# Performance work log

Measured on AMD Instinct MI355X. Metric: run time of the kernel, lower is better.

Reference implementation:

```python
import jax, jax.numpy as jnp
import numpy as np

DIM = 4096
HIDDEN = 11008
B, S = 4, 2048


def setup_inputs() -> dict:
    key = jax.random.key(0)
    k_x, k_g, k_u, k_d = jax.random.split(key, 4)
    x = jax.random.normal(k_x, (B, S, DIM), dtype=jnp.float32)
    # int8-range quantized weights, stored as int32 per spec (values in [-127, 127])
    w_gate = jax.random.randint(k_g, (HIDDEN, DIM), -127, 128, dtype=jnp.int32)
    w_up = jax.random.randint(k_u, (HIDDEN, DIM), -127, 128, dtype=jnp.int32)
    w_down = jax.random.randint(k_d, (DIM, HIDDEN), -127, 128, dtype=jnp.int32)
    # per-tensor scales (realistic small magnitudes)
    scale_gate = jnp.float32(0.01)
    scale_up = jnp.float32(0.01)
    scale_down = jnp.float32(0.01)
    return {
        "x": x,
        "w_gate": w_gate,
        "w_up": w_up,
        "w_down": w_down,
        "scale_gate": scale_gate,
        "scale_up": scale_up,
        "scale_down": scale_down,
    }


def _qlinear(x, w_int, scale):
    # faithful to QuantizedLinear.forward: dequantize then F.linear (x @ w.T)
    w = w_int.astype(x.dtype) * scale
    return jnp.einsum("bsd,hd->bsh", x, w)


def reference(x, w_gate, w_up, w_down, scale_gate, scale_up, scale_down):
    x_gate = _qlinear(x, w_gate, scale_gate)      # [B,S,HIDDEN]
    x_up = _qlinear(x, w_up, scale_up)            # [B,S,HIDDEN]
    x_mid = jax.nn.silu(x_gate) * x_up            # SwiGLU
    x_out = _qlinear(x_mid, w_down, scale_down)   # [B,S,DIM]
    return x_out
```

## Files before the change

kernel.cpp:

```cpp
#include <hip/hip_runtime.h>
#include <hip/hip_bf16.h>
#include <cstdint>
#include <cstddef>

#define DIM 4096
#define HIDDEN 11008
#define MTOK 8192

typedef __bf16 bf16x8 __attribute__((ext_vector_type(8)));
typedef float floatx4 __attribute__((ext_vector_type(4)));

__device__ __forceinline__ unsigned short f2bf(float f) {
    union { float f; unsigned int u; } v; v.f = f;
    unsigned int r = v.u + 0x7FFFu + ((v.u >> 16) & 1u);
    return (unsigned short)(r >> 16);
}

__device__ __forceinline__ void gload16(const void* g, void* l) {
    __builtin_amdgcn_global_load_lds(
        (const __attribute__((address_space(1))) unsigned int*)g,
        (__attribute__((address_space(3))) unsigned int*)l,
        16, 0, 0);
}

__device__ __forceinline__ floatx4 mfma16(bf16x8 a, bf16x8 b, floatx4 c) {
    return __builtin_amdgcn_mfma_f32_16x16x32_bf16(a, b, c, 0, 0, 0);
}


__global__ void cvt_f32_bf16(const float4* __restrict__ in, ushort4* __restrict__ out, int n4) {
    int i = blockIdx.x * 256 + threadIdx.x;
    if (i < n4) {
        float4 v = in[i];
        ushort4 o;
        o.x = f2bf(v.x); o.y = f2bf(v.y); o.z = f2bf(v.z); o.w = f2bf(v.w);
        out[i] = o;
    }
}

__global__ void cvt_i32_bf16(const int4* __restrict__ in, ushort4* __restrict__ out, int n4) {
    int i = blockIdx.x * 256 + threadIdx.x;
    if (i < n4) {
        int4 v = in[i];
        ushort4 o;
        o.x = f2bf((float)v.x); o.y = f2bf((float)v.y);
        o.z = f2bf((float)v.z); o.w = f2bf((float)v.w);
        out[i] = o;
    }
}

__global__ __launch_bounds__(256) void gemm_gateup(
    const unsigned short* __restrict__ A,
    const unsigned short* __restrict__ Bg,
    const unsigned short* __restrict__ Bu,
    unsigned short* __restrict__ mid,
    const float* __restrict__ sgp, const float* __restrict__ sup)
{
    __shared__ __align__(16) unsigned short sA[128 * 32];
    __shared__ __align__(16) unsigned short sBg[64 * 32];
    __shared__ __align__(16) unsigned short sBu[64 * 32];

    const int tid  = threadIdx.x;
    const int lane = tid & 63;
    const int wave = tid >> 6;
    const int wr   = wave >> 1;
    const int wc   = wave & 1;
    const int quad = lane >> 4;
    const int l16  = lane & 15;

    const size_t m0 = (size_t)blockIdx.x * 128;
    const size_t n0 = (size_t)blockIdx.y * 64;

    const int srow = tid >> 2;
    const int scol = (tid & 3) * 8;

    const unsigned short* gA0 = A  + (m0 + srow) * DIM + scol;
    const unsigned short* gA1 = gA0 + (size_t)64 * DIM;
    const unsigned short* gBg = Bg + (n0 + srow) * DIM + scol;
    const unsigned short* gBu = Bu + (n0 + srow) * DIM + scol;

    unsigned short* lA0 = &sA[tid * 8];
    unsigned short* lA1 = &sA[(tid + 256) * 8];
    unsigned short* lBg = &sBg[tid * 8];
    unsigned short* lBu = &sBu[tid * 8];

    const unsigned short* rA[4];
    const unsigned short* rBg[2];
    const unsigned short* rBu[2];
    for (int i = 0; i < 4; ++i)
        rA[i] = &sA[(wr * 64 + i * 16 + l16) * 32 + quad * 8];
    for (int j = 0; j < 2; ++j) {
        rBg[j] = &sBg[(wc * 32 + j * 16 + l16) * 32 + quad * 8];
        rBu[j] = &sBu[(wc * 32 + j * 16 + l16) * 32 + quad * 8];
    }

    floatx4 accg[4][2], accu[4][2];
    const floatx4 zero = {0.f, 0.f, 0.f, 0.f};
    for (int i = 0; i < 4; ++i)
        for (int j = 0; j < 2; ++j) { accg[i][j] = zero; accu[i][j] = zero; }

    for (int kt = 0; kt < DIM / 32; ++kt) {
        __syncthreads();
        gload16(gA0, lA0);
        gload16(gA1, lA1);
        gload16(gBg, lBg);
        gload16(gBu, lBu);
        gA0 += 32; gA1 += 32; gBg += 32; gBu += 32;
        __syncthreads();

        bf16x8 af[4], bg[2], bu[2];
        for (int i = 0; i < 4; ++i) af[i] = *(const bf16x8*)rA[i];
        for (int j = 0; j < 2; ++j) {
            bg[j] = *(const bf16x8*)rBg[j];
            bu[j] = *(const bf16x8*)rBu[j];
        }
        for (int i = 0; i < 4; ++i)
            for (int j = 0; j < 2; ++j) {
                accg[i][j] = mfma16(af[i], bg[j], accg[i][j]);
                accu[i][j] = mfma16(af[i], bu[j], accu[i][j]);
            }
    }

    const float s_g = *sgp;
    const float s_u = *sup;
    for (int i = 0; i < 4; ++i) {
        const size_t row = m0 + wr * 64 + i * 16 + quad * 4;
        for (int j = 0; j < 2; ++j) {
            const size_t col = n0 + wc * 32 + j * 16 + l16;
            for (int r = 0; r < 4; ++r) {
                float g = accg[i][j][r] * s_g;
                float u = accu[i][j][r] * s_u;
                float sig = 1.0f / (1.0f + __expf(-g));
                float v = g * sig * u;
                mid[(row + r) * HIDDEN + col] = f2bf(v);
            }
        }
    }
}

__global__ __launch_bounds__(256) void gemm_down(
    const unsigned short* __restrict__ A,
    const unsigned short* __restrict__ B,
    float* __restrict__ out,
    const float* __restrict__ sdp)
{
    __shared__ __align__(16) unsigned short sA[128 * 32];
    __shared__ __align__(16) unsigned short sB[128 * 32];

    const int tid  = threadIdx.x;
    const int lane = tid & 63;
    const int wave = tid >> 6;
    const int wr   = wave >> 1;
    const int wc   = wave & 1;
    const int quad = lane >> 4;
    const int l16  = lane & 15;

    const size_t m0 = (size_t)blockIdx.x * 128;
    const size_t n0 = (size_t)blockIdx.y * 128;

    const int srow = tid >> 2;
    const int scol = (tid & 3) * 8;

    const unsigned short* gA0 = A + (m0 + srow) * HIDDEN + scol;
    const unsigned short* gA1 = gA0 + (size_t)64 * HIDDEN;
    const unsigned short* gB0 = B + (n0 + srow) * HIDDEN + scol;
    const unsigned short* gB1 = gB0 + (size_t)64 * HIDDEN;

    unsigned short* lA0 = &sA[tid * 8];
    unsigned short* lA1 = &sA[(tid + 256) * 8];
    unsigned short* lB0 = &sB[tid * 8];
    unsigned short* lB1 = &sB[(tid + 256) * 8];

    const unsigned short* rA[4];
    const unsigned short* rB[4];
    for (int i = 0; i < 4; ++i) {
        rA[i] = &sA[(wr * 64 + i * 16 + l16) * 32 + quad * 8];
        rB[i] = &sB[(wc * 64 + i * 16 + l16) * 32 + quad * 8];
    }

    floatx4 acc[4][4];
    const floatx4 zero = {0.f, 0.f, 0.f, 0.f};
    for (int i = 0; i < 4; ++i)
        for (int j = 0; j < 4; ++j) acc[i][j] = zero;

    for (int kt = 0; kt < HIDDEN / 32; ++kt) {
        __syncthreads();
        gload16(gA0, lA0);
        gload16(gA1, lA1);
        gload16(gB0, lB0);
        gload16(gB1, lB1);
        gA0 += 32; gA1 += 32; gB0 += 32; gB1 += 32;
        __syncthreads();

        bf16x8 af[4], bf[4];
        for (int i = 0; i < 4; ++i) {
            af[i] = *(const bf16x8*)rA[i];
            bf[i] = *(const bf16x8*)rB[i];
        }
        for (int i = 0; i < 4; ++i)
            for (int j = 0; j < 4; ++j)
                acc[i][j] = mfma16(af[i], bf[j], acc[i][j]);
    }

    const float s_d = *sdp;
    for (int i = 0; i < 4; ++i) {
        const size_t row = m0 + wr * 64 + i * 16 + quad * 4;
        for (int j = 0; j < 4; ++j) {
            const size_t col = n0 + wc * 64 + j * 16 + l16;
            for (int r = 0; r < 4; ++r)
                out[(row + r) * DIM + col] = acc[i][j][r] * s_d;
        }
    }
}


extern "C" void kernel_launch(void* const* d_in, const int* in_sizes, int n_in,
                              void* d_out, int out_size, void* d_ws, size_t ws_size,
                              hipStream_t stream) {
    const float* x  = (const float*)d_in[0];
    const int*   wg = (const int*)d_in[1];
    const int*   wu = (const int*)d_in[2];
    const int*   wd = (const int*)d_in[3];
    const float* sg = (const float*)d_in[4];
    const float* su = (const float*)d_in[5];
    const float* sd = (const float*)d_in[6];
    float* out = (float*)d_out;

    unsigned short* xb   = (unsigned short*)d_ws;
    unsigned short* wgb  = xb  + (size_t)MTOK * DIM;
    unsigned short* wub  = wgb + (size_t)HIDDEN * DIM;
    unsigned short* wdb  = wub + (size_t)HIDDEN * DIM;
    unsigned short* midb = wdb + (size_t)DIM * HIDDEN;

    {
        int n4 = MTOK * DIM / 4;
        cvt_f32_bf16<<<dim3((n4 + 255) / 256), 256, 0, stream>>>((const float4*)x, (ushort4*)xb, n4);
    }
    {
        int n4 = HIDDEN * DIM / 4;
        cvt_i32_bf16<<<dim3((n4 + 255) / 256), 256, 0, stream>>>((const int4*)wg, (ushort4*)wgb, n4);
        cvt_i32_bf16<<<dim3((n4 + 255) / 256), 256, 0, stream>>>((const int4*)wu, (ushort4*)wub, n4);
        cvt_i32_bf16<<<dim3((n4 + 255) / 256), 256, 0, stream>>>((const int4*)wd, (ushort4*)wdb, n4);
    }

    gemm_gateup<<<dim3(MTOK / 128, HIDDEN / 64), 256, 0, stream>>>(xb, wgb, wub, midb, sg, su);

    gemm_down<<<dim3(MTOK / 128, DIM / 128), 256, 0, stream>>>(midb, wdb, out, sd);
}
```

Baseline: 3.171 ms.

## Load GEMM fragments directly from global into registers with double buffering

```diff
diff --git a/kernel.cpp b/kernel.cpp
--- a/kernel.cpp
+++ b/kernel.cpp
@@ -14,13 +14,6 @@
     union { float f; unsigned int u; } v; v.f = f;
     unsigned int r = v.u + 0x7FFFu + ((v.u >> 16) & 1u);
     return (unsigned short)(r >> 16);
-}
-
-__device__ __forceinline__ void gload16(const void* g, void* l) {
-    __builtin_amdgcn_global_load_lds(
-        (const __attribute__((address_space(1))) unsigned int*)g,
-        (__attribute__((address_space(3))) unsigned int*)l,
-        16, 0, 0);
 }
 
 __device__ __forceinline__ floatx4 mfma16(bf16x8 a, bf16x8 b, floatx4 c) {
@@ -56,10 +49,6 @@
     unsigned short* __restrict__ mid,
     const float* __restrict__ sgp, const float* __restrict__ sup)
 {
-    __shared__ __align__(16) unsigned short sA[128 * 32];
-    __shared__ __align__(16) unsigned short sBg[64 * 32];
-    __shared__ __align__(16) unsigned short sBu[64 * 32];
-
     const int tid  = threadIdx.x;
     const int lane = tid & 63;
     const int wave = tid >> 6;
@@ -71,27 +60,15 @@
     const size_t m0 = (size_t)blockIdx.x * 128;
     const size_t n0 = (size_t)blockIdx.y * 64;
 
-    const int srow = tid >> 2;
-    const int scol = (tid & 3) * 8;
-
-    const unsigned short* gA0 = A  + (m0 + srow) * DIM + scol;
-    const unsigned short* gA1 = gA0 + (size_t)64 * DIM;
-    const unsigned short* gBg = Bg + (n0 + srow) * DIM + scol;
-    const unsigned short* gBu = Bu + (n0 + srow) * DIM + scol;
-
-    unsigned short* lA0 = &sA[tid * 8];
-    unsigned short* lA1 = &sA[(tid + 256) * 8];
-    unsigned short* lBg = &sBg[tid * 8];
-    unsigned short* lBu = &sBu[tid * 8];
-
-    const unsigned short* rA[4];
-    const unsigned short* rBg[2];
-    const unsigned short* rBu[2];
+    const unsigned short* pA[4];
+    const unsigned short* pG[2];
+    const unsigned short* pU[2];
     for (int i = 0; i < 4; ++i)
-        rA[i] = &sA[(wr * 64 + i * 16 + l16) * 32 + quad * 8];
+        pA[i] = A + (m0 + wr * 64 + i * 16 + l16) * DIM + quad * 8;
     for (int j = 0; j < 2; ++j) {
-        rBg[j] = &sBg[(wc * 32 + j * 16 + l16) * 32 + quad * 8];
-        rBu[j] = &sBu[(wc * 32 + j * 16 + l16) * 32 + quad * 8];
+        const size_t row = n0 + wc * 32 + j * 16 + l16;
+        pG[j] = Bg + row * DIM + quad * 8;
+        pU[j] = Bu + row * DIM + quad * 8;
     }
 
     floatx4 accg[4][2], accu[4][2];
@@ -99,25 +76,28 @@
     for (int i = 0; i < 4; ++i)
         for (int j = 0; j < 2; ++j) { accg[i][j] = zero; accu[i][j] = zero; }
 
-    for (int kt = 0; kt < DIM / 32; ++kt) {
-        __syncthreads();
-        gload16(gA0, lA0);
-        gload16(gA1, lA1);
-        gload16(gBg, lBg);
-        gload16(gBu, lBu);
-        gA0 += 32; gA1 += 32; gBg += 32; gBu += 32;
-        __syncthreads();
-
-        bf16x8 af[4], bg[2], bu[2];
-        for (int i = 0; i < 4; ++i) af[i] = *(const bf16x8*)rA[i];
+    constexpr int NK = DIM / 32;
+
+    bf16x8 fA[2][4], fG[2][2], fU[2][2];
+    for (int i = 0; i < 4; ++i) fA[0][i] = *(const bf16x8*)pA[i];
+    for (int j = 0; j < 2; ++j) {
+        fG[0][j] = *(const bf16x8*)pG[j];
+        fU[0][j] = *(const bf16x8*)pU[j];
+    }
+
+    #pragma unroll 2
+    for (int kt = 0; kt < NK; ++kt) {
+        const int cur = kt & 1, nxt = cur ^ 1;
+        const size_t off = (size_t)((kt + 1 < NK) ? (kt + 1) : kt) * 32;
+        for (int i = 0; i < 4; ++i) fA[nxt][i] = *(const bf16x8*)(pA[i] + off);
         for (int j = 0; j < 2; ++j) {
-            bg[j] = *(const bf16x8*)rBg[j];
-            bu[j] = *(const bf16x8*)rBu[j];
+            fG[nxt][j] = *(const bf16x8*)(pG[j] + off);
+            fU[nxt][j] = *(const bf16x8*)(pU[j] + off);
         }
         for (int i = 0; i < 4; ++i)
             for (int j = 0; j < 2; ++j) {
-                accg[i][j] = mfma16(af[i], bg[j], accg[i][j]);
-                accu[i][j] = mfma16(af[i], bu[j], accu[i][j]);
+                accg[i][j] = mfma16(fA[cur][i], fG[cur][j], accg[i][j]);
+                accu[i][j] = mfma16(fA[cur][i], fU[cur][j], accu[i][j]);
             }
     }
 
@@ -144,9 +124,6 @@
     float* __restrict__ out,
     const float* __restrict__ sdp)
 {
-    __shared__ __align__(16) unsigned short sA[128 * 32];
-    __shared__ __align__(16) unsigned short sB[128 * 32];
-
     const int tid  = threadIdx.x;
     const int lane = tid & 63;
     const int wave = tid >> 6;
@@ -158,24 +135,11 @@
     const size_t m0 = (size_t)blockIdx.x * 128;
     const size_t n0 = (size_t)blockIdx.y * 128;
 
-    const int srow = tid >> 2;
-    const int scol = (tid & 3) * 8;
-
-    const unsigned short* gA0 = A + (m0 + srow) * HIDDEN + scol;
-    const unsigned short* gA1 = gA0 + (size_t)64 * HIDDEN;
-    const unsigned short* gB0 = B + (n0 + srow) * HIDDEN + scol;
-    const unsigned short* gB1 = gB0 + (size_t)64 * HIDDEN;
-
-    unsigned short* lA0 = &sA[tid * 8];
-    unsigned short* lA1 = &sA[(tid + 256) * 8];
-    unsigned short* lB0 = &sB[tid * 8];
-    unsigned short* lB1 = &sB[(tid + 256) * 8];
-
-    const unsigned short* rA[4];
-    const unsigned short* rB[4];
-    for (int i = 0; i < 4; ++i) {
-        rA[i] = &sA[(wr * 64 + i * 16 + l16) * 32 + quad * 8];
-        rB[i] = &sB[(wc * 64 + i * 16 + l16) * 32 + quad * 8];
+    const unsigned short* pA[4];
+    const unsigned short* pB[4];
+    for (int i = 0; i < 4; ++i) {
+        pA[i] = A + (m0 + wr * 64 + i * 16 + l16) * HIDDEN + quad * 8;
+        pB[i] = B + (n0 + wc * 64 + i * 16 + l16) * HIDDEN + quad * 8;
     }
 
     floatx4 acc[4][4];
@@ -183,23 +147,25 @@
     for (int i = 0; i < 4; ++i)
         for (int j = 0; j < 4; ++j) acc[i][j] = zero;
 
-    for (int kt = 0; kt < HIDDEN / 32; ++kt) {
-        __syncthreads();
-        gload16(gA0, lA0);
-        gload16(gA1, lA1);
-        gload16(gB0, lB0);
-        gload16(gB1, lB1);
-        gA0 += 32; gA1 += 32; gB0 += 32; gB1 += 32;
-        __syncthreads();
-
-        bf16x8 af[4], bf[4];
+    constexpr int NK = HIDDEN / 32;
+
+    bf16x8 fA[2][4], fB[2][4];
+    for (int i = 0; i < 4; ++i) {
+        fA[0][i] = *(const bf16x8*)pA[i];
+        fB[0][i] = *(const bf16x8*)pB[i];
+    }
+
+    #pragma unroll 2
+    for (int kt = 0; kt < NK; ++kt) {
+        const int cur = kt & 1, nxt = cur ^ 1;
+        const size_t off = (size_t)((kt + 1 < NK) ? (kt + 1) : kt) * 32;
         for (int i = 0; i < 4; ++i) {
-            af[i] = *(const bf16x8*)rA[i];
-            bf[i] = *(const bf16x8*)rB[i];
+            fA[nxt][i] = *(const bf16x8*)(pA[i] + off);
+            fB[nxt][i] = *(const bf16x8*)(pB[i] + off);
         }
         for (int i = 0; i < 4; ++i)
             for (int j = 0; j < 4; ++j)
-                acc[i][j] = mfma16(af[i], bf[j], acc[i][j]);
+                acc[i][j] = mfma16(fA[cur][i], fB[cur][j], acc[i][j]);
     }
 
     const float s_d = *sdp;
```

Measured after the change: 7.922 ms. 150% more time.
